# Optimization experiments

Hardware: AMD Instinct MI355X
Metric: run time of the kernel (lower is better)

The kernel has to match this reference:

```python
import jax, jax.numpy as jnp
import numpy as np

N_LAYERS = 3
NUM_USERS = 100_000
NUM_ITEMS = 100_000
EMB_DIM = 64
NNZ = 2_000_000


def setup_inputs() -> dict:
    key = jax.random.key(0)
    k1, k2, k3, k4, k5 = jax.random.split(key, 5)
    n_nodes = NUM_USERS + 1 + NUM_ITEMS  # 200001
    user_emb = jax.random.normal(k1, (NUM_USERS + 1, EMB_DIM), dtype=jnp.float32) * 0.1
    user_emb = user_emb.at[0].set(0.0)  # padding_idx=0
    item_emb = jax.random.normal(k2, (NUM_ITEMS + 1, EMB_DIM), dtype=jnp.float32) * 0.1
    item_emb = item_emb.at[0].set(0.0)  # padding_idx=0
    adj_rows = jax.random.randint(k3, (NNZ,), 0, n_nodes, dtype=jnp.int32)
    adj_cols = jax.random.randint(k4, (NNZ,), 0, n_nodes, dtype=jnp.int32)
    # symmetric-normalized adjacency values are small positive numbers
    adj_vals = jax.random.uniform(k5, (NNZ,), dtype=jnp.float32) * 0.1
    return {
        "user_emb": user_emb,
        "item_emb": item_emb,
        "adj_rows": adj_rows,
        "adj_cols": adj_cols,
        "adj_vals": adj_vals,
    }


def _spmm(adj_rows, adj_cols, adj_vals, x, n_nodes):
    # y[r] = sum over nnz with row==r of val * x[col]  (COO SpMM)
    msgs = adj_vals[:, None] * x[adj_cols]  # [nnz, d]
    return jax.ops.segment_sum(msgs, adj_rows, num_segments=n_nodes)


def reference(user_emb, item_emb, adj_rows, adj_cols, adj_vals):
    n_users_p1 = user_emb.shape[0]
    all_emb = jnp.concatenate([user_emb, item_emb[1:]], axis=0)  # [N, d]
    n_nodes = all_emb.shape[0]
    acc = all_emb  # running sum for layer-mean pooling
    x = all_emb
    for _ in range(N_LAYERS):
        x = _spmm(adj_rows, adj_cols, adj_vals, x, n_nodes)
        acc = acc + x
    all_out = acc / jnp.asarray(N_LAYERS + 1, all_emb.dtype)
    user_out = all_out[:n_users_p1]
    item_out = jnp.concatenate(
        [jnp.zeros((1, all_out.shape[1]), all_out.dtype), all_out[n_users_p1:]], axis=0
    )
    return user_out, item_out
```

## Files before the change

kernel.cpp:

```cpp
#include <hip/hip_runtime.h>


#define N_NODES 200001
#define NUP1    100001
#define D       64
#define DV      16
#define DV8     8
#define CHUNK   512
#define NCHUNK  ((N_NODES + CHUNK - 1) / CHUNK)
#define T_TILE  4096
#define EPT     16
#define CAP     6144

__device__ __forceinline__ unsigned short f2bf(float f) {
  unsigned u = __float_as_uint(f);
  unsigned r = (u + 0x7FFFu + ((u >> 16) & 1u)) >> 16;
  return (unsigned short)r;
}
__device__ __forceinline__ float bf2f(unsigned short h) {
  return __uint_as_float(((unsigned)h) << 16);
}
__device__ __forceinline__ float bflo(unsigned u) { return __uint_as_float(u << 16); }
__device__ __forceinline__ float bfhi(unsigned u) { return __uint_as_float(u & 0xFFFF0000u); }

__global__ __launch_bounds__(256) void init_kernel(
    const float4* __restrict__ user_emb,
    const float4* __restrict__ item_emb,
    ushort4* __restrict__ x0,
    int* __restrict__ bucket_cnt) {
  int idx = blockIdx.x * 256 + threadIdx.x;
  if (idx < NCHUNK) bucket_cnt[idx] = 0;
  if (idx >= N_NODES * DV) return;
  int n = idx >> 4;
  int j = idx & 15;
  float4 v = (n < NUP1) ? user_emb[idx]
                        : item_emb[(size_t)(n - 100000) * DV + j];
  x0[idx] = make_ushort4(f2bf(v.x), f2bf(v.y), f2bf(v.z), f2bf(v.w));
}

__global__ __launch_bounds__(256) void pass1_bucket(
    const int*   __restrict__ rows,
    const int*   __restrict__ cols,
    const float* __restrict__ vals,
    int*  __restrict__ bucket_cnt,
    int2* __restrict__ bucket_arr,
    int nnz) {
  __shared__ int lcount[NCHUNK];
  __shared__ int lbase[NCHUNK];
  int t = threadIdx.x;
  for (int i = t; i < NCHUNK; i += 256) lcount[i] = 0;
  __syncthreads();
  long base = (long)blockIdx.x * T_TILE;
  int2 pk[EPT];
  int  meta[EPT];
#pragma unroll
  for (int k = 0; k < EPT; ++k) {
    long e = base + t + (long)k * 256;
    if (e < nnz) {
      int r = rows[e];
      int b = r >> 9;
      int rank = atomicAdd(&lcount[b], 1);
      pk[k] = make_int2(((r & 511) << 18) | cols[e], __float_as_int(vals[e]));
      meta[k] = (rank << 9) | b;
    } else {
      meta[k] = -1;
    }
  }
  __syncthreads();
  for (int b = t; b < NCHUNK; b += 256) {
    int c = lcount[b];
    lbase[b] = (c > 0) ? (b * CAP + atomicAdd(&bucket_cnt[b], c)) : 0;
  }
  __syncthreads();
#pragma unroll
  for (int k = 0; k < EPT; ++k) {
    if (meta[k] >= 0) {
      int b = meta[k] & 511;
      int rank = meta[k] >> 9;
      bucket_arr[lbase[b] + rank] = pk[k];
    }
  }
}

__global__ __launch_bounds__(512) void scan_chunks_kernel(
    const int* __restrict__ cnt, int* __restrict__ off,
    int* __restrict__ row_ptr, int nnz) {
  __shared__ int sh[512];
  int t = threadIdx.x;
  int v = (t < NCHUNK) ? cnt[t] : 0;
  sh[t] = v;
  __syncthreads();
  for (int o = 1; o < 512; o <<= 1) {
    int u = (t >= o) ? sh[t - o] : 0;
    __syncthreads();
    sh[t] += u;
    __syncthreads();
  }
  if (t < NCHUNK) off[t] = sh[t] - v;
  if (t == 0) row_ptr[N_NODES] = nnz;
}

__global__ __launch_bounds__(256) void build_csr_chunk(
    const int*  __restrict__ bucket_cnt,
    const int2* __restrict__ bucket_arr,
    const int*  __restrict__ chunk_off,
    int*  __restrict__ row_ptr,
    int2* __restrict__ edge_s) {
  __shared__ int lcnt[CHUNK];
  __shared__ int tsum[256];
  int b = blockIdx.x, t = threadIdx.x;
  lcnt[t] = 0; lcnt[t + 256] = 0;
  __syncthreads();
  int ne = bucket_cnt[b];
  const int2* ba = bucket_arr + (size_t)b * CAP;
  for (int i = t; i < ne; i += 256)
    atomicAdd(&lcnt[ba[i].x >> 18], 1);
  __syncthreads();
  int base = t * 2;
  int l0 = lcnt[base], l1 = lcnt[base + 1];
  int s = l0 + l1;
  tsum[t] = s;
  __syncthreads();
  for (int o = 1; o < 256; o <<= 1) {
    int v = (t >= o) ? tsum[t - o] : 0;
    __syncthreads();
    tsum[t] += v;
    __syncthreads();
  }
  int run = tsum[t] - s + chunk_off[b];
  int row0 = b * CHUNK;
  if (row0 + base < N_NODES) row_ptr[row0 + base] = run;
  lcnt[base] = run;
  run += l0;
  if (row0 + base + 1 < N_NODES) row_ptr[row0 + base + 1] = run;
  lcnt[base + 1] = run;
  __syncthreads();
  for (int i = t; i < ne; i += 256) {
    int2 ed = ba[i];
    int p = atomicAdd(&lcnt[ed.x >> 18], 1);
    edge_s[p] = make_int2(ed.x & 0x3FFFF, ed.y);
  }
}

__global__ __launch_bounds__(256) void spmm_bf16_kernel(
    const int*  __restrict__ row_ptr,
    const int2* __restrict__ edge_s,
    const uint4* __restrict__ x,
    uint4*       __restrict__ y) {
  int t = blockIdx.x * 256 + threadIdx.x;
  int r = t >> 3;
  int j = t & 7;
  if (r >= N_NODES) return;
  int s = row_ptr[r];
  int e = row_ptr[r + 1];
  float a0 = 0.f, a1 = 0.f, a2 = 0.f, a3 = 0.f;
  float a4 = 0.f, a5 = 0.f, a6 = 0.f, a7 = 0.f;
  int last = e - 1;
#define ACCUM(V, XV) {                                    \
    a0 += (V) * bflo((XV).x); a1 += (V) * bfhi((XV).x);   \
    a2 += (V) * bflo((XV).y); a3 += (V) * bfhi((XV).y);   \
    a4 += (V) * bflo((XV).z); a5 += (V) * bfhi((XV).z);   \
    a6 += (V) * bflo((XV).w); a7 += (V) * bfhi((XV).w); }
  for (int g = s; g < e; g += 8) {
    int2 e0 = edge_s[min(g + 0, last)];
    int2 e1 = edge_s[min(g + 1, last)];
    int2 e2 = edge_s[min(g + 2, last)];
    int2 e3 = edge_s[min(g + 3, last)];
    int2 e4 = edge_s[min(g + 4, last)];
    int2 e5 = edge_s[min(g + 5, last)];
    int2 e6 = edge_s[min(g + 6, last)];
    int2 e7 = edge_s[min(g + 7, last)];
    uint4 x0 = x[(size_t)e0.x * DV8 + j];
    uint4 x1 = x[(size_t)e1.x * DV8 + j];
    uint4 x2 = x[(size_t)e2.x * DV8 + j];
    uint4 x3 = x[(size_t)e3.x * DV8 + j];
    uint4 x4 = x[(size_t)e4.x * DV8 + j];
    uint4 x5 = x[(size_t)e5.x * DV8 + j];
    uint4 x6 = x[(size_t)e6.x * DV8 + j];
    uint4 x7 = x[(size_t)e7.x * DV8 + j];
    float v0 = __int_as_float(e0.y);
    float v1 = (g + 1 < e) ? __int_as_float(e1.y) : 0.f;
    float v2 = (g + 2 < e) ? __int_as_float(e2.y) : 0.f;
    float v3 = (g + 3 < e) ? __int_as_float(e3.y) : 0.f;
    float v4 = (g + 4 < e) ? __int_as_float(e4.y) : 0.f;
    float v5 = (g + 5 < e) ? __int_as_float(e5.y) : 0.f;
    float v6 = (g + 6 < e) ? __int_as_float(e6.y) : 0.f;
    float v7 = (g + 7 < e) ? __int_as_float(e7.y) : 0.f;
    ACCUM(v0, x0); ACCUM(v1, x1); ACCUM(v2, x2); ACCUM(v3, x3);
    ACCUM(v4, x4); ACCUM(v5, x5); ACCUM(v6, x6); ACCUM(v7, x7);
  }
#undef ACCUM
  uint4 o;
  o.x = ((unsigned)f2bf(a1) << 16) | f2bf(a0);
  o.y = ((unsigned)f2bf(a3) << 16) | f2bf(a2);
  o.z = ((unsigned)f2bf(a5) << 16) | f2bf(a4);
  o.w = ((unsigned)f2bf(a7) << 16) | f2bf(a6);
  y[t] = o;
}

__global__ __launch_bounds__(256) void final_kernel(
    const float4*  __restrict__ user_emb,
    const float4*  __restrict__ item_emb,
    const ushort4* __restrict__ y1,
    const ushort4* __restrict__ y2,
    const ushort4* __restrict__ y3,
    float4* __restrict__ out) {
  int idx = blockIdx.x * 256 + threadIdx.x;
  if (idx < DV) {
    out[(size_t)NUP1 * DV + idx] = make_float4(0.f, 0.f, 0.f, 0.f);
  }
  if (idx >= N_NODES * DV) return;
  int n = idx >> 4;
  int j = idx & 15;
  float4 v = (n < NUP1) ? user_emb[idx]
                        : item_emb[(size_t)(n - 100000) * DV + j];
  ushort4 a = y1[idx], b = y2[idx], c = y3[idx];
  float4 o;
  o.x = 0.25f * (v.x + bf2f(a.x) + bf2f(b.x) + bf2f(c.x));
  o.y = 0.25f * (v.y + bf2f(a.y) + bf2f(b.y) + bf2f(c.y));
  o.z = 0.25f * (v.z + bf2f(a.z) + bf2f(b.z) + bf2f(c.z));
  o.w = 0.25f * (v.w + bf2f(a.w) + bf2f(b.w) + bf2f(c.w));
  int rm = (n < NUP1) ? n : n + 1;
  out[(size_t)rm * DV + j] = o;
}

static inline char* align16(char* p) {
  return (char*)(((uintptr_t)p + 15) & ~(uintptr_t)15);
}

extern "C" void kernel_launch(void* const* d_in, const int* in_sizes, int n_in,
                              void* d_out, int out_size, void* d_ws, size_t ws_size,
                              hipStream_t stream) {
  const float* user_emb = (const float*)d_in[0];
  const float* item_emb = (const float*)d_in[1];
  const int*   rows     = (const int*)d_in[2];
  const int*   cols     = (const int*)d_in[3];
  const float* vals     = (const float*)d_in[4];
  const int    nnz      = in_sizes[2];

  const size_t xbytes = (size_t)N_NODES * D * sizeof(unsigned short);
  char* p = (char*)d_ws;
  ushort4* x0 = (ushort4*)p;  p += xbytes;
  ushort4* y1 = (ushort4*)p;  p += xbytes;
  ushort4* y2 = (ushort4*)p;  p += xbytes;
  ushort4* y3 = (ushort4*)p;  p += xbytes;
  int2* bucket_arr = (int2*)y2;
  p = align16(p);
  int2* edge_s = (int2*)p;    p += (size_t)nnz * sizeof(int2);
  p = align16(p);
  int* row_ptr = (int*)p;     p += (size_t)(N_NODES + 1) * sizeof(int);
  p = align16(p);
  int* chunk_off = (int*)p;   p += (size_t)NCHUNK * sizeof(int);
  p = align16(p);
  int* bucket_cnt = (int*)p;  p += (size_t)NCHUNK * sizeof(int);

  float* out = (float*)d_out;

  const int row_elems = N_NODES * DV;
  const int node_grid = (row_elems + 255) / 256;
  const int spmm_grid = (N_NODES * DV8 + 255) / 256;
  const int tile_grid = (nnz + T_TILE - 1) / T_TILE;

  init_kernel<<<node_grid, 256, 0, stream>>>(
      (const float4*)user_emb, (const float4*)item_emb, x0, bucket_cnt);
  pass1_bucket<<<tile_grid, 256, 0, stream>>>(
      rows, cols, vals, bucket_cnt, bucket_arr, nnz);
  scan_chunks_kernel<<<1, 512, 0, stream>>>(bucket_cnt, chunk_off, row_ptr, nnz);
  build_csr_chunk<<<NCHUNK, 256, 0, stream>>>(
      bucket_cnt, bucket_arr, chunk_off, row_ptr, edge_s);

  spmm_bf16_kernel<<<spmm_grid, 256, 0, stream>>>(
      row_ptr, edge_s, (const uint4*)x0, (uint4*)y1);
  spmm_bf16_kernel<<<spmm_grid, 256, 0, stream>>>(
      row_ptr, edge_s, (const uint4*)y1, (uint4*)y2);
  spmm_bf16_kernel<<<spmm_grid, 256, 0, stream>>>(
      row_ptr, edge_s, (const uint4*)y2, (uint4*)y3);

  final_kernel<<<node_grid, 256, 0, stream>>>(
      (const float4*)user_emb, (const float4*)item_emb, y1, y2, y3,
      (float4*)out);
}
```

Measured before the change: 323.2 us.

## Fuse final pooling into last SpMM and split bucket counters into padded replicas

The third SpMM now computes the layer-mean pooling directly: it reads the original fp32 embeddings plus the bf16 y1 and y2 rows and writes fp32 output, so the y3 buffer and the separate final kernel are gone. The bucketing pass also splits each chunk's global atomic counter into two replicas chosen by block parity, padded to separate cache lines. Each replica gets half of the chunk's bucket capacity, which reduces atomic contention. The CSR build and the scan read both halves. Risk: a half-capacity region (3072 entries) could overflow for a dense chunk, and the fused kernel writes with a less regular output pattern.

```diff
diff --git a/kernel.cpp b/kernel.cpp
--- a/kernel.cpp
+++ b/kernel.cpp
@@ -11,6 +11,10 @@
 #define T_TILE  4096
 #define EPT     16
 #define CAP     6144
+#define REP     2
+#define HALFCAP (CAP / REP)
+#define CNT_STRIDE 16
+#define CNT_TOTAL  (NCHUNK * REP * CNT_STRIDE)
 
 __device__ __forceinline__ unsigned short f2bf(float f) {
   unsigned u = __float_as_uint(f);
@@ -29,7 +33,7 @@
     ushort4* __restrict__ x0,
     int* __restrict__ bucket_cnt) {
   int idx = blockIdx.x * 256 + threadIdx.x;
-  if (idx < NCHUNK) bucket_cnt[idx] = 0;
+  if (idx < CNT_TOTAL) bucket_cnt[idx] = 0;
   if (idx >= N_NODES * DV) return;
   int n = idx >> 4;
   int j = idx & 15;
@@ -51,6 +55,7 @@
   for (int i = t; i < NCHUNK; i += 256) lcount[i] = 0;
   __syncthreads();
   long base = (long)blockIdx.x * T_TILE;
+  int rep = blockIdx.x & (REP - 1);
   int2 pk[EPT];
   int  meta[EPT];
 #pragma unroll
@@ -69,7 +74,10 @@
   __syncthreads();
   for (int b = t; b < NCHUNK; b += 256) {
     int c = lcount[b];
-    lbase[b] = (c > 0) ? (b * CAP + atomicAdd(&bucket_cnt[b], c)) : 0;
+    lbase[b] = (c > 0)
+        ? (b * CAP + rep * HALFCAP +
+           atomicAdd(&bucket_cnt[(b * REP + rep) * CNT_STRIDE], c))
+        : 0;
   }
   __syncthreads();
 #pragma unroll
@@ -87,7 +95,9 @@
     int* __restrict__ row_ptr, int nnz) {
   __shared__ int sh[512];
   int t = threadIdx.x;
-  int v = (t < NCHUNK) ? cnt[t] : 0;
+  int v = (t < NCHUNK)
+      ? cnt[(t * REP + 0) * CNT_STRIDE] + cnt[(t * REP + 1) * CNT_STRIDE]
+      : 0;
   sh[t] = v;
   __syncthreads();
   for (int o = 1; o < 512; o <<= 1) {
@@ -111,10 +121,13 @@
   int b = blockIdx.x, t = threadIdx.x;
   lcnt[t] = 0; lcnt[t + 256] = 0;
   __syncthreads();
-  int ne = bucket_cnt[b];
+  int ne0 = bucket_cnt[(b * REP + 0) * CNT_STRIDE];
+  int ne1 = bucket_cnt[(b * REP + 1) * CNT_STRIDE];
   const int2* ba = bucket_arr + (size_t)b * CAP;
-  for (int i = t; i < ne; i += 256)
+  for (int i = t; i < ne0; i += 256)
     atomicAdd(&lcnt[ba[i].x >> 18], 1);
+  for (int i = t; i < ne1; i += 256)
+    atomicAdd(&lcnt[ba[HALFCAP + i].x >> 18], 1);
   __syncthreads();
   int base = t * 2;
   int l0 = lcnt[base], l1 = lcnt[base + 1];
@@ -135,61 +148,71 @@
   if (row0 + base + 1 < N_NODES) row_ptr[row0 + base + 1] = run;
   lcnt[base + 1] = run;
   __syncthreads();
-  for (int i = t; i < ne; i += 256) {
+  for (int i = t; i < ne0; i += 256) {
     int2 ed = ba[i];
     int p = atomicAdd(&lcnt[ed.x >> 18], 1);
     edge_s[p] = make_int2(ed.x & 0x3FFFF, ed.y);
   }
-}
+  for (int i = t; i < ne1; i += 256) {
+    int2 ed = ba[HALFCAP + i];
+    int p = atomicAdd(&lcnt[ed.x >> 18], 1);
+    edge_s[p] = make_int2(ed.x & 0x3FFFF, ed.y);
+  }
+}
+
+#define SPMM_BODY                                                   \
+  int t = blockIdx.x * 256 + threadIdx.x;                           \
+  int r = t >> 3;                                                   \
+  int j = t & 7;                                                    \
+  float a0 = 0.f, a1 = 0.f, a2 = 0.f, a3 = 0.f;                     \
+  float a4 = 0.f, a5 = 0.f, a6 = 0.f, a7 = 0.f;                     \
+  {                                                                 \
+    int s = row_ptr[r];                                             \
+    int e = row_ptr[r + 1];                                         \
+    int last = e - 1;                                               \
+    for (int g = s; g < e; g += 8) {                                \
+      int2 e0 = edge_s[min(g + 0, last)];                           \
+      int2 e1 = edge_s[min(g + 1, last)];                           \
+      int2 e2 = edge_s[min(g + 2, last)];                           \
+      int2 e3 = edge_s[min(g + 3, last)];                           \
+      int2 e4 = edge_s[min(g + 4, last)];                           \
+      int2 e5 = edge_s[min(g + 5, last)];                           \
+      int2 e6 = edge_s[min(g + 6, last)];                           \
+      int2 e7 = edge_s[min(g + 7, last)];                           \
+      uint4 x0 = x[(size_t)e0.x * DV8 + j];                         \
+      uint4 x1 = x[(size_t)e1.x * DV8 + j];                         \
+      uint4 x2 = x[(size_t)e2.x * DV8 + j];                         \
+      uint4 x3 = x[(size_t)e3.x * DV8 + j];                         \
+      uint4 x4 = x[(size_t)e4.x * DV8 + j];                         \
+      uint4 x5 = x[(size_t)e5.x * DV8 + j];                         \
+      uint4 x6 = x[(size_t)e6.x * DV8 + j];                         \
+      uint4 x7 = x[(size_t)e7.x * DV8 + j];                         \
+      float v0 = __int_as_float(e0.y);                              \
+      float v1 = (g + 1 < e) ? __int_as_float(e1.y) : 0.f;          \
+      float v2 = (g + 2 < e) ? __int_as_float(e2.y) : 0.f;          \
+      float v3 = (g + 3 < e) ? __int_as_float(e3.y) : 0.f;          \
+      float v4 = (g + 4 < e) ? __int_as_float(e4.y) : 0.f;          \
+      float v5 = (g + 5 < e) ? __int_as_float(e5.y) : 0.f;          \
+      float v6 = (g + 6 < e) ? __int_as_float(e6.y) : 0.f;          \
+      float v7 = (g + 7 < e) ? __int_as_float(e7.y) : 0.f;          \
+      ACCUM(v0, x0); ACCUM(v1, x1); ACCUM(v2, x2); ACCUM(v3, x3);   \
+      ACCUM(v4, x4); ACCUM(v5, x5); ACCUM(v6, x6); ACCUM(v7, x7);   \
+    }                                                               \
+  }
+
+#define ACCUM(V, XV) {                                    \
+    a0 += (V) * bflo((XV).x); a1 += (V) * bfhi((XV).x);   \
+    a2 += (V) * bflo((XV).y); a3 += (V) * bfhi((XV).y);   \
+    a4 += (V) * bflo((XV).z); a5 += (V) * bfhi((XV).z);   \
+    a6 += (V) * bflo((XV).w); a7 += (V) * bfhi((XV).w); }
 
 __global__ __launch_bounds__(256) void spmm_bf16_kernel(
     const int*  __restrict__ row_ptr,
     const int2* __restrict__ edge_s,
     const uint4* __restrict__ x,
     uint4*       __restrict__ y) {
-  int t = blockIdx.x * 256 + threadIdx.x;
-  int r = t >> 3;
-  int j = t & 7;
-  if (r >= N_NODES) return;
-  int s = row_ptr[r];
-  int e = row_ptr[r + 1];
-  float a0 = 0.f, a1 = 0.f, a2 = 0.f, a3 = 0.f;
-  float a4 = 0.f, a5 = 0.f, a6 = 0.f, a7 = 0.f;
-  int last = e - 1;
-#define ACCUM(V, XV) {                                    \
-    a0 += (V) * bflo((XV).x); a1 += (V) * bfhi((XV).x);   \
-    a2 += (V) * bflo((XV).y); a3 += (V) * bfhi((XV).y);   \
-    a4 += (V) * bflo((XV).z); a5 += (V) * bfhi((XV).z);   \
-    a6 += (V) * bflo((XV).w); a7 += (V) * bfhi((XV).w); }
-  for (int g = s; g < e; g += 8) {
-    int2 e0 = edge_s[min(g + 0, last)];
-    int2 e1 = edge_s[min(g + 1, last)];
-    int2 e2 = edge_s[min(g + 2, last)];
-    int2 e3 = edge_s[min(g + 3, last)];
-    int2 e4 = edge_s[min(g + 4, last)];
-    int2 e5 = edge_s[min(g + 5, last)];
-    int2 e6 = edge_s[min(g + 6, last)];
-    int2 e7 = edge_s[min(g + 7, last)];
-    uint4 x0 = x[(size_t)e0.x * DV8 + j];
-    uint4 x1 = x[(size_t)e1.x * DV8 + j];
-    uint4 x2 = x[(size_t)e2.x * DV8 + j];
-    uint4 x3 = x[(size_t)e3.x * DV8 + j];
-    uint4 x4 = x[(size_t)e4.x * DV8 + j];
-    uint4 x5 = x[(size_t)e5.x * DV8 + j];
-    uint4 x6 = x[(size_t)e6.x * DV8 + j];
-    uint4 x7 = x[(size_t)e7.x * DV8 + j];
-    float v0 = __int_as_float(e0.y);
-    float v1 = (g + 1 < e) ? __int_as_float(e1.y) : 0.f;
-    float v2 = (g + 2 < e) ? __int_as_float(e2.y) : 0.f;
-    float v3 = (g + 3 < e) ? __int_as_float(e3.y) : 0.f;
-    float v4 = (g + 4 < e) ? __int_as_float(e4.y) : 0.f;
-    float v5 = (g + 5 < e) ? __int_as_float(e5.y) : 0.f;
-    float v6 = (g + 6 < e) ? __int_as_float(e6.y) : 0.f;
-    float v7 = (g + 7 < e) ? __int_as_float(e7.y) : 0.f;
-    ACCUM(v0, x0); ACCUM(v1, x1); ACCUM(v2, x2); ACCUM(v3, x3);
-    ACCUM(v4, x4); ACCUM(v5, x5); ACCUM(v6, x6); ACCUM(v7, x7);
-  }
-#undef ACCUM
+  if ((blockIdx.x * 256 + threadIdx.x) >> 3 >= N_NODES) return;
+  SPMM_BODY
   uint4 o;
   o.x = ((unsigned)f2bf(a1) << 16) | f2bf(a0);
   o.y = ((unsigned)f2bf(a3) << 16) | f2bf(a2);
@@ -198,31 +221,44 @@
   y[t] = o;
 }
 
-__global__ __launch_bounds__(256) void final_kernel(
-    const float4*  __restrict__ user_emb,
-    const float4*  __restrict__ item_emb,
-    const ushort4* __restrict__ y1,
-    const ushort4* __restrict__ y2,
-    const ushort4* __restrict__ y3,
+__global__ __launch_bounds__(256) void spmm_final_kernel(
+    const int*  __restrict__ row_ptr,
+    const int2* __restrict__ edge_s,
+    const uint4* __restrict__ x,
+    const uint4* __restrict__ y1u,
+    const float4* __restrict__ user_emb,
+    const float4* __restrict__ item_emb,
     float4* __restrict__ out) {
-  int idx = blockIdx.x * 256 + threadIdx.x;
-  if (idx < DV) {
-    out[(size_t)NUP1 * DV + idx] = make_float4(0.f, 0.f, 0.f, 0.f);
-  }
-  if (idx >= N_NODES * DV) return;
-  int n = idx >> 4;
-  int j = idx & 15;
-  float4 v = (n < NUP1) ? user_emb[idx]
-                        : item_emb[(size_t)(n - 100000) * DV + j];
-  ushort4 a = y1[idx], b = y2[idx], c = y3[idx];
-  float4 o;
-  o.x = 0.25f * (v.x + bf2f(a.x) + bf2f(b.x) + bf2f(c.x));
-  o.y = 0.25f * (v.y + bf2f(a.y) + bf2f(b.y) + bf2f(c.y));
-  o.z = 0.25f * (v.z + bf2f(a.z) + bf2f(b.z) + bf2f(c.z));
-  o.w = 0.25f * (v.w + bf2f(a.w) + bf2f(b.w) + bf2f(c.w));
-  int rm = (n < NUP1) ? n : n + 1;
-  out[(size_t)rm * DV + j] = o;
-}
+  int gt = blockIdx.x * 256 + threadIdx.x;
+  if (gt < DV) out[(size_t)NUP1 * DV + gt] = make_float4(0.f, 0.f, 0.f, 0.f);
+  if (gt >> 3 >= N_NODES) return;
+  SPMM_BODY
+  uint4 w1 = y1u[(size_t)r * DV8 + j];
+  uint4 w2 = x  [(size_t)r * DV8 + j];
+  int rm = (r < NUP1) ? r : r + 1;
+  size_t eb = (size_t)r * DV + 2 * j;
+  float4 f0, f1;
+  if (r < NUP1) {
+    f0 = user_emb[eb];
+    f1 = user_emb[eb + 1];
+  } else {
+    size_t ib = (size_t)(r - 100000) * DV + 2 * j;
+    f0 = item_emb[ib];
+    f1 = item_emb[ib + 1];
+  }
+  float4 o0, o1;
+  o0.x = 0.25f * (f0.x + bflo(w1.x) + bflo(w2.x) + a0);
+  o0.y = 0.25f * (f0.y + bfhi(w1.x) + bfhi(w2.x) + a1);
+  o0.z = 0.25f * (f0.z + bflo(w1.y) + bflo(w2.y) + a2);
+  o0.w = 0.25f * (f0.w + bfhi(w1.y) + bfhi(w2.y) + a3);
+  o1.x = 0.25f * (f1.x + bflo(w1.z) + bflo(w2.z) + a4);
+  o1.y = 0.25f * (f1.y + bfhi(w1.z) + bfhi(w2.z) + a5);
+  o1.z = 0.25f * (f1.z + bflo(w1.w) + bflo(w2.w) + a6);
+  o1.w = 0.25f * (f1.w + bfhi(w1.w) + bfhi(w2.w) + a7);
+  out[(size_t)rm * DV + 2 * j]     = o0;
+  out[(size_t)rm * DV + 2 * j + 1] = o1;
+}
+#undef ACCUM
 
 static inline char* align16(char* p) {
   return (char*)(((uintptr_t)p + 15) & ~(uintptr_t)15);
@@ -245,6 +281,7 @@
   ushort4* y2 = (ushort4*)p;  p += xbytes;
   ushort4* y3 = (ushort4*)p;  p += xbytes;
   int2* bucket_arr = (int2*)y2;
+  (void)y3;
   p = align16(p);
   int2* edge_s = (int2*)p;    p += (size_t)nnz * sizeof(int2);
   p = align16(p);
@@ -252,7 +289,7 @@
   p = align16(p);
   int* chunk_off = (int*)p;   p += (size_t)NCHUNK * sizeof(int);
   p = align16(p);
-  int* bucket_cnt = (int*)p;  p += (size_t)NCHUNK * sizeof(int);
+  int* bucket_cnt = (int*)p;  p += (size_t)CNT_TOTAL * sizeof(int);
 
   float* out = (float*)d_out;
 
@@ -273,10 +310,7 @@
       row_ptr, edge_s, (const uint4*)x0, (uint4*)y1);
   spmm_bf16_kernel<<<spmm_grid, 256, 0, stream>>>(
       row_ptr, edge_s, (const uint4*)y1, (uint4*)y2);
-  spmm_bf16_kernel<<<spmm_grid, 256, 0, stream>>>(
-      row_ptr, edge_s, (const uint4*)y2, (uint4*)y3);
-
-  final_kernel<<<node_grid, 256, 0, stream>>>(
-      (const float4*)user_emb, (const float4*)item_emb, y1, y2, y3,
-      (float4*)out);
-}
+  spmm_final_kernel<<<spmm_grid, 256, 0, stream>>>(
+      row_ptr, edge_s, (const uint4*)y2, (const uint4*)y1,
+      (const float4*)user_emb, (const float4*)item_emb, (float4*)out);
+}
```

Result: faster. 312.8 us (-3.2%).
